# Performance work log

Measured on AMD Instinct MI355X. Metric: run time of the kernel, lower is better.

## Reference

```python
import jax, jax.numpy as jnp
import numpy as np

VOCAB_SIZE = 32000
PAD_IDX = 0


def setup_inputs() -> dict:
    key = jax.random.key(0)
    k1, k2 = jax.random.split(key)
    tokens = jax.random.randint(k1, (256, 2048), 0, VOCAB_SIZE, dtype=jnp.int64 if jax.config.jax_enable_x64 else jnp.int32)
    lengths = jax.random.randint(k2, (256,), 0, 2048, dtype=tokens.dtype)
    return {"tokens": tokens, "lengths": lengths}


def reference(tokens, lengths):
    # Faithful to torch OneHotEncoder.forward:
    #   onehot[b,t,:] = one_hot(tokens[b,t]) with pad_idx column zeroed per position,
    #   then summed over t -> counts [batch, vocab]. NOTE: the torch code computes a
    #   clamped `outhot` but RETURNS the un-clamped `onehot` counts; we match that.
    # Efficient form: direct per-row scatter-add histogram, skipping pad tokens,
    # without materializing the [B, T, V] intermediate.
    B, T = tokens.shape
    rows = jnp.arange(B)[:, None]  # [B,1] broadcasts against tokens [B,T]
    contrib = jnp.where(tokens == PAD_IDX, 0.0, 1.0).astype(jnp.float32)
    counts = jnp.zeros((B, VOCAB_SIZE), dtype=jnp.float32).at[rows, tokens].add(contrib)
    # pad_idx column is always zeroed (scatter of 0 at pad_selector per position)
    counts = counts.at[:, PAD_IDX].set(0.0)
    return counts
```

## Files before the change

### kernel.cpp

```cpp
#include <hip/hip_runtime.h>


#define VOCAB  32000
#define CHUNKS 4
#define CV     (VOCAB / CHUNKS)
#define BLOCK  256

typedef float f32x4 __attribute__((ext_vector_type(4)));

__global__ __launch_bounds__(BLOCK)
void OneHotEncoder_43052752175267_kernel(const int* __restrict__ tokens,
                                         float* __restrict__ out,
                                         int T) {
    __shared__ __align__(16) unsigned int hist[CV / 2];

    const int row   = blockIdx.x >> 2;
    const int chunk = blockIdx.x & (CHUNKS - 1);
    const int lo    = chunk * CV;
    const int tid   = threadIdx.x;

    uint4* h4 = (uint4*)hist;
    const uint4 z = make_uint4(0u, 0u, 0u, 0u);
    for (int i = tid; i < CV / 8; i += BLOCK)
        h4[i] = z;
    __syncthreads();

    const int* trow = tokens + (long long)row * T;
    for (int i = tid; i < T; i += BLOCK) {
        int tok = trow[i];
        unsigned local = (unsigned)(tok - lo);
        if (tok != 0 && local < (unsigned)CV)
            atomicAdd(&hist[local >> 1], 1u << ((local & 1) << 4));
    }
    __syncthreads();

    f32x4* o4 = (f32x4*)(out + (long long)row * VOCAB + lo);
    const uint2* h2 = (const uint2*)hist;
    for (int i = tid; i < CV / 4; i += BLOCK) {
        uint2 h = h2[i];
        f32x4 f;
        f.x = (float)(h.x & 0xFFFFu);
        f.y = (float)(h.x >> 16);
        f.z = (float)(h.y & 0xFFFFu);
        f.w = (float)(h.y >> 16);
        __builtin_nontemporal_store(f, &o4[i]);
    }
}

extern "C" void kernel_launch(void* const* d_in, const int* in_sizes, int n_in,
                              void* d_out, int out_size, void* d_ws, size_t ws_size,
                              hipStream_t stream) {
    const int* tokens = (const int*)d_in[0];
    const int B = in_sizes[1];
    const int T = in_sizes[0] / B;
    float* out = (float*)d_out;

    OneHotEncoder_43052752175267_kernel<<<dim3(B * CHUNKS), dim3(BLOCK), 0, stream>>>(tokens, out, T);
}
```

Before: 69.05 us.

## Replace LDS histogram with global zero-fill plus global atomic scatter

Drops the per-row shared-memory histogram, where each row was split into four vocab chunks that each re-read the whole token row. Instead, one kernel zero-fills the output with vector stores and a second kernel does float atomicAdd directly into global memory for each non-pad token. The aim is to avoid re-reading tokens and to remove the LDS zero-and-convert pass. In exchange there are two launches and many global atomics, and the output is written twice: once by the zero fill and again by scattered atomics.

```diff
diff --git a/kernel.cpp b/kernel.cpp
--- a/kernel.cpp
+++ b/kernel.cpp
@@ -1,50 +1,44 @@
 #include <hip/hip_runtime.h>
 
 
-#define VOCAB  32000
-#define CHUNKS 4
-#define CV     (VOCAB / CHUNKS)
-#define BLOCK  256
+#define VOCAB 32000
+#define BLOCK 256
 
 typedef float f32x4 __attribute__((ext_vector_type(4)));
 
 __global__ __launch_bounds__(BLOCK)
-void OneHotEncoder_43052752175267_kernel(const int* __restrict__ tokens,
-                                         float* __restrict__ out,
-                                         int T) {
-    __shared__ __align__(16) unsigned int hist[CV / 2];
+void OneHotEncoder_43052752175267_zero(float* __restrict__ out, int n4) {
+    f32x4* o4 = (f32x4*)out;
+    const f32x4 z = {0.f, 0.f, 0.f, 0.f};
+    const int stride = gridDim.x * BLOCK;
+    for (int i = blockIdx.x * BLOCK + threadIdx.x; i < n4; i += stride)
+        o4[i] = z;
+}
 
-    const int row   = blockIdx.x >> 2;
-    const int chunk = blockIdx.x & (CHUNKS - 1);
-    const int lo    = chunk * CV;
-    const int tid   = threadIdx.x;
+__global__ __launch_bounds__(BLOCK)
+void OneHotEncoder_43052752175267_scatter4(const int* __restrict__ tokens,
+                                           float* __restrict__ out,
+                                           int T, int total4) {
+    const int idx = blockIdx.x * BLOCK + threadIdx.x;
+    if (idx >= total4) return;
+    const int4 t = ((const int4*)tokens)[idx];
+    const int row = (idx * 4) / T;
+    float* orow = out + (long long)row * VOCAB;
+    if (t.x != 0) atomicAdd(&orow[t.x], 1.0f);
+    if (t.y != 0) atomicAdd(&orow[t.y], 1.0f);
+    if (t.z != 0) atomicAdd(&orow[t.z], 1.0f);
+    if (t.w != 0) atomicAdd(&orow[t.w], 1.0f);
+}
 
-    uint4* h4 = (uint4*)hist;
-    const uint4 z = make_uint4(0u, 0u, 0u, 0u);
-    for (int i = tid; i < CV / 8; i += BLOCK)
-        h4[i] = z;
-    __syncthreads();
-
-    const int* trow = tokens + (long long)row * T;
-    for (int i = tid; i < T; i += BLOCK) {
-        int tok = trow[i];
-        unsigned local = (unsigned)(tok - lo);
-        if (tok != 0 && local < (unsigned)CV)
-            atomicAdd(&hist[local >> 1], 1u << ((local & 1) << 4));
-    }
-    __syncthreads();
-
-    f32x4* o4 = (f32x4*)(out + (long long)row * VOCAB + lo);
-    const uint2* h2 = (const uint2*)hist;
-    for (int i = tid; i < CV / 4; i += BLOCK) {
-        uint2 h = h2[i];
-        f32x4 f;
-        f.x = (float)(h.x & 0xFFFFu);
-        f.y = (float)(h.x >> 16);
-        f.z = (float)(h.y & 0xFFFFu);
-        f.w = (float)(h.y >> 16);
-        __builtin_nontemporal_store(f, &o4[i]);
-    }
+__global__ __launch_bounds__(BLOCK)
+void OneHotEncoder_43052752175267_scatter1(const int* __restrict__ tokens,
+                                           float* __restrict__ out,
+                                           int T, int total) {
+    const int idx = blockIdx.x * BLOCK + threadIdx.x;
+    if (idx >= total) return;
+    const int tok = tokens[idx];
+    if (tok != 0)
+        atomicAdd(&out[(long long)(idx / T) * VOCAB + tok], 1.0f);
 }
 
 extern "C" void kernel_launch(void* const* d_in, const int* in_sizes, int n_in,
@@ -55,5 +49,19 @@
     const int T = in_sizes[0] / B;
     float* out = (float*)d_out;
 
-    OneHotEncoder_43052752175267_kernel<<<dim3(B * CHUNKS), dim3(BLOCK), 0, stream>>>(tokens, out, T);
+    const int n4 = (B * VOCAB) / 4;
+    const int zgrid = 2048;
+    OneHotEncoder_43052752175267_zero<<<dim3(zgrid), dim3(BLOCK), 0, stream>>>(out, n4);
+
+    const int total = B * T;
+    if ((T & 3) == 0) {
+        const int total4 = total / 4;
+        const int sgrid = (total4 + BLOCK - 1) / BLOCK;
+        OneHotEncoder_43052752175267_scatter4<<<dim3(sgrid), dim3(BLOCK), 0, stream>>>(
+            tokens, out, T, total4);
+    } else {
+        const int sgrid = (total + BLOCK - 1) / BLOCK;
+        OneHotEncoder_43052752175267_scatter1<<<dim3(sgrid), dim3(BLOCK), 0, stream>>>(
+            tokens, out, T, total);
+    }
 }
```

New measurement: 92.72 us. 34.3% more time.
